# Kernel tuning notes

Hardware: AMD Instinct MI355X
Metric: run time of the kernel (lower is better)

Reference implementation:

```python
import jax, jax.numpy as jnp
import numpy as np
import math

DT = 1.0
BETA = 15.0
TAU0 = 3.0
THRESHOLD = 0.25


def setup_inputs() -> dict:
    key = jax.random.key(0)
    B, F, L = 64, 256, 2048
    I = jax.random.normal(key, (B, F, L), dtype=jnp.float32)
    raw0 = math.log(math.expm1(TAU0))
    raw_tau = jnp.full((F,), raw0, dtype=jnp.float32)
    thr = jnp.float32(THRESHOLD)
    return {"I": I, "raw_tau": raw_tau, "thr": thr}


def reference(I, raw_tau, thr):
    B, F, L = I.shape
    tau = jax.nn.softplus(raw_tau) + 1e-4          # [F]
    alpha = jnp.exp(-DT / tau).astype(I.dtype)      # [F] decay per filter

    def step(v, I_t):
        # v: [B, F], I_t: [B, F]
        v_pre = alpha * v + (1.0 - alpha) * I_t
        z = BETA * (v_pre - thr)
        s = (v_pre >= thr).astype(I.dtype)
        v_new = v_pre * (1.0 - s)                   # hard reset on spike
        return v_new, (z, s)

    I_time = jnp.moveaxis(I, -1, 0)                 # [L, B, F]
    v0 = jnp.zeros((B, F), dtype=I.dtype)
    _, (z_hist, s_hist) = jax.lax.scan(step, v0, I_time)
    # back to [B, F, L]
    return jnp.moveaxis(z_hist, 0, -1), jnp.moveaxis(s_hist, 0, -1)
```

## Files before the change

### kernel.cpp

```cpp
#include <hip/hip_runtime.h>
#include <cmath>

#define LIF_L 2048
#define LIF_F 256
#define LIF_B 64
#define LIF_BF (LIF_B * LIF_F)
#define TT 64
#define NTILE (LIF_L / TT)
#define STR 65

__global__ __launch_bounds__(64) void lif_scan_kernel(
    const float* __restrict__ I, const float* __restrict__ raw_tau,
    const float* __restrict__ thr_p, float* __restrict__ out) {
#pragma clang fp contract(off)
  __shared__ float ldsI[64 * STR];
  __shared__ float ldsZ[64 * STR];
  __shared__ float ldsS[64 * STR];

  const int lane = threadIdx.x;
  const int cbase = blockIdx.x * 64;
  const int q = lane >> 4;
  const int m = lane & 15;

  const int f = (cbase + lane) & (LIF_F - 1);
  const double rt = (double)raw_tau[f];
  const double sp = (rt > 0.0) ? (rt + log1p(exp(-rt))) : log1p(exp(rt));
  const float alpha = (float)exp(-1.0 / (sp + 1e-4));
  const float oma = 1.0f - alpha;
  const float thr = thr_p[0];
  const float beta = 15.0f;

  const float4* __restrict__ Ip = (const float4*)I;
  float4* __restrict__ Zp = (float4*)out;
  float4* __restrict__ Sp = (float4*)(out + (size_t)LIF_BF * LIF_L);

  float v = 0.0f;
  float4 inbuf[16];

#pragma unroll
  for (int k = 0; k < 16; ++k) {
    const int row = 4 * k + q;
    inbuf[k] = Ip[(size_t)(cbase + row) * (LIF_L / 4) + m];
  }

  for (int tile = 0; tile < NTILE; ++tile) {
#pragma unroll
    for (int k = 0; k < 16; ++k) {
      const int row = 4 * k + q;
      float* p = &ldsI[row * STR + 4 * m];
      p[0] = inbuf[k].x; p[1] = inbuf[k].y; p[2] = inbuf[k].z; p[3] = inbuf[k].w;
    }
    const int tn = (tile + 1 < NTILE) ? tile + 1 : tile;
#pragma unroll
    for (int k = 0; k < 16; ++k) {
      const int row = 4 * k + q;
      inbuf[k] = Ip[(size_t)(cbase + row) * (LIF_L / 4) + tn * (TT / 4) + m];
    }
    __builtin_amdgcn_wave_barrier();

    float* rowI = &ldsI[lane * STR];
    float* rowZ = &ldsZ[lane * STR];
    float* rowS = &ldsS[lane * STR];
#pragma unroll 8
    for (int t = 0; t < TT; ++t) {
      const float in = rowI[t];
      const float vpre = alpha * v + oma * in;
      rowZ[t] = beta * (vpre - thr);
      rowS[t] = (vpre >= thr) ? 1.0f : 0.0f;
      v = (vpre >= thr) ? 0.0f : vpre;
    }
    __builtin_amdgcn_wave_barrier();

#pragma unroll
    for (int k = 0; k < 16; ++k) {
      const int row = 4 * k + q;
      const size_t oidx = (size_t)(cbase + row) * (LIF_L / 4) + tile * (TT / 4) + m;
      const float* pz = &ldsZ[row * STR + 4 * m];
      float4 zv = {pz[0], pz[1], pz[2], pz[3]};
      Zp[oidx] = zv;
      const float* ps = &ldsS[row * STR + 4 * m];
      float4 sv = {ps[0], ps[1], ps[2], ps[3]};
      Sp[oidx] = sv;
    }
    __builtin_amdgcn_wave_barrier();
  }
}

extern "C" void kernel_launch(void* const* d_in, const int* in_sizes, int n_in,
                              void* d_out, int out_size, void* d_ws,
                              size_t ws_size, hipStream_t stream) {
  const float* I = (const float*)d_in[0];
  const float* raw_tau = (const float*)d_in[1];
  const float* thr = (const float*)d_in[2];
  float* out = (float*)d_out;
  dim3 grid(LIF_BF / 64), block(64);
  lif_scan_kernel<<<grid, block, 0, stream>>>(I, raw_tau, thr, out);
}
```

Measured before the change: 386.1 us.

## Widen time tile, store only v_pre in LDS, derive z/s at writeback

Doubles the time tile to 128 steps so each wave has twice as many loads in flight per prefetch. LDS now holds float4 rows, and only v_pre is staged instead of separate z and s buffers. The z and s outputs are computed from v_pre in the coalesced writeback loop, which removes per-step LDS stores and moves that arithmetic off the serial recurrence. The cost is more registers for the larger prefetch buffer, roughly the same LDS footprint, and launch bounds that pin occupancy hints.

```diff
diff --git a/kernel.cpp b/kernel.cpp
--- a/kernel.cpp
+++ b/kernel.cpp
@@ -5,17 +5,17 @@
 #define LIF_F 256
 #define LIF_B 64
 #define LIF_BF (LIF_B * LIF_F)
-#define TT 64
-#define NTILE (LIF_L / TT)
-#define STR 65
+#define TT 128
+#define NT (LIF_L / TT)
+#define W4 (TT / 4)
+#define S4 (W4 + 1)
 
-__global__ __launch_bounds__(64) void lif_scan_kernel(
+__global__ __launch_bounds__(64, 1) void lif_scan_kernel(
     const float* __restrict__ I, const float* __restrict__ raw_tau,
     const float* __restrict__ thr_p, float* __restrict__ out) {
 #pragma clang fp contract(off)
-  __shared__ float ldsI[64 * STR];
-  __shared__ float ldsZ[64 * STR];
-  __shared__ float ldsS[64 * STR];
+  __shared__ float4 ldsI[64 * S4];
+  __shared__ float4 ldsV[64 * S4];
 
   const int lane = threadIdx.x;
   const int cbase = blockIdx.x * 64;
@@ -35,52 +35,67 @@
   float4* __restrict__ Sp = (float4*)(out + (size_t)LIF_BF * LIF_L);
 
   float v = 0.0f;
-  float4 inbuf[16];
+  float4 inbuf[32];
 
 #pragma unroll
   for (int k = 0; k < 16; ++k) {
-    const int row = 4 * k + q;
-    inbuf[k] = Ip[(size_t)(cbase + row) * (LIF_L / 4) + m];
+    const size_t rb = (size_t)(cbase + 4 * k + q) * (LIF_L / 4);
+    inbuf[2 * k] = Ip[rb + m];
+    inbuf[2 * k + 1] = Ip[rb + m + 16];
   }
 
-  for (int tile = 0; tile < NTILE; ++tile) {
+  for (int tile = 0; tile < NT; ++tile) {
 #pragma unroll
     for (int k = 0; k < 16; ++k) {
       const int row = 4 * k + q;
-      float* p = &ldsI[row * STR + 4 * m];
-      p[0] = inbuf[k].x; p[1] = inbuf[k].y; p[2] = inbuf[k].z; p[3] = inbuf[k].w;
+      ldsI[row * S4 + m] = inbuf[2 * k];
+      ldsI[row * S4 + m + 16] = inbuf[2 * k + 1];
     }
-    const int tn = (tile + 1 < NTILE) ? tile + 1 : tile;
+    if (tile + 1 < NT) {
 #pragma unroll
-    for (int k = 0; k < 16; ++k) {
-      const int row = 4 * k + q;
-      inbuf[k] = Ip[(size_t)(cbase + row) * (LIF_L / 4) + tn * (TT / 4) + m];
+      for (int k = 0; k < 16; ++k) {
+        const size_t rb =
+            (size_t)(cbase + 4 * k + q) * (LIF_L / 4) + (tile + 1) * W4;
+        inbuf[2 * k] = Ip[rb + m];
+        inbuf[2 * k + 1] = Ip[rb + m + 16];
+      }
     }
     __builtin_amdgcn_wave_barrier();
 
-    float* rowI = &ldsI[lane * STR];
-    float* rowZ = &ldsZ[lane * STR];
-    float* rowS = &ldsS[lane * STR];
+    const float4* rI = &ldsI[lane * S4];
+    float4* rV = &ldsV[lane * S4];
 #pragma unroll 8
-    for (int t = 0; t < TT; ++t) {
-      const float in = rowI[t];
-      const float vpre = alpha * v + oma * in;
-      rowZ[t] = beta * (vpre - thr);
-      rowS[t] = (vpre >= thr) ? 1.0f : 0.0f;
-      v = (vpre >= thr) ? 0.0f : vpre;
+    for (int u = 0; u < W4; ++u) {
+      const float4 in = rI[u];
+      float4 vp;
+      vp.x = alpha * v + oma * in.x;
+      v = (vp.x >= thr) ? 0.0f : vp.x;
+      vp.y = alpha * v + oma * in.y;
+      v = (vp.y >= thr) ? 0.0f : vp.y;
+      vp.z = alpha * v + oma * in.z;
+      v = (vp.z >= thr) ? 0.0f : vp.z;
+      vp.w = alpha * v + oma * in.w;
+      v = (vp.w >= thr) ? 0.0f : vp.w;
+      rV[u] = vp;
     }
     __builtin_amdgcn_wave_barrier();
 
 #pragma unroll
     for (int k = 0; k < 16; ++k) {
       const int row = 4 * k + q;
-      const size_t oidx = (size_t)(cbase + row) * (LIF_L / 4) + tile * (TT / 4) + m;
-      const float* pz = &ldsZ[row * STR + 4 * m];
-      float4 zv = {pz[0], pz[1], pz[2], pz[3]};
-      Zp[oidx] = zv;
-      const float* ps = &ldsS[row * STR + 4 * m];
-      float4 sv = {ps[0], ps[1], ps[2], ps[3]};
-      Sp[oidx] = sv;
+      const size_t rb = (size_t)(cbase + row) * (LIF_L / 4) + tile * W4;
+#pragma unroll
+      for (int h = 0; h < 2; ++h) {
+        const int col = m + 16 * h;
+        const float4 vp = ldsV[row * S4 + col];
+        float4 z, s;
+        z.x = beta * (vp.x - thr); s.x = (vp.x >= thr) ? 1.0f : 0.0f;
+        z.y = beta * (vp.y - thr); s.y = (vp.y >= thr) ? 1.0f : 0.0f;
+        z.z = beta * (vp.z - thr); s.z = (vp.z >= thr) ? 1.0f : 0.0f;
+        z.w = beta * (vp.w - thr); s.w = (vp.w >= thr) ? 1.0f : 0.0f;
+        Zp[rb + col] = z;
+        Sp[rb + col] = s;
+      }
     }
     __builtin_amdgcn_wave_barrier();
   }
```

After: 407.3 us. 1.05x slower.
